# Optimization experiments

Measured on AMD Instinct MI355X. Metric: run time of the kernel, lower is better.

## Reference

```python
import jax, jax.numpy as jnp
import numpy as np
import math

DIM_Q = 512; DIM_K = 512; DIM_V = 512; H = 8; EPS = 1e-5

def _layernorm(x, g, b):
    mu = jnp.mean(x, axis=-1, keepdims=True)
    var = jnp.mean((x - mu) ** 2, axis=-1, keepdims=True)
    return (x - mu) * jax.lax.rsqrt(var + EPS) * g + b

def setup_inputs() -> dict:
    key = jax.random.key(0)
    ks = jax.random.split(key, 12)
    B, NQ, NK = 8, 1024, 1024
    s = 0.02
    return {
        "Q": jax.random.normal(ks[0], (B, NQ, DIM_Q), jnp.float32),
        "K": jax.random.normal(ks[1], (B, NK, DIM_K), jnp.float32),
        "attention_mask": jax.random.randint(ks[2], (B, NK), 0, 2, jnp.int32),
        "Wq": jax.random.normal(ks[3], (DIM_Q, DIM_V), jnp.float32) * s,
        "bq": jnp.zeros((DIM_V,), jnp.float32),
        "Wk": jax.random.normal(ks[4], (DIM_K, DIM_V), jnp.float32) * s,
        "bk": jnp.zeros((DIM_V,), jnp.float32),
        "Wv": jax.random.normal(ks[5], (DIM_K, DIM_V), jnp.float32) * s,
        "bv": jnp.zeros((DIM_V,), jnp.float32),
        "Wo": jax.random.normal(ks[6], (DIM_V, DIM_V), jnp.float32) * s,
        "bo": jnp.zeros((DIM_V,), jnp.float32),
        "g0": jnp.ones((DIM_V,), jnp.float32),
        "b0": jnp.zeros((DIM_V,), jnp.float32),
        "g1": jnp.ones((DIM_V,), jnp.float32),
        "b1": jnp.zeros((DIM_V,), jnp.float32),
    }

def reference(Q, K, attention_mask, Wq, bq, Wk, bk, Wv, bv, Wo, bo, g0, b0, g1, b1):
    B, NQ, _ = Q.shape
    NK = K.shape[1]
    dh = DIM_V // H
    q = (Q @ Wq + bq).reshape(B, NQ, H, dh).transpose(0, 2, 1, 3)  # (B,H,NQ,dh)
    k = (K @ Wk + bk).reshape(B, NK, H, dh).transpose(0, 2, 1, 3)
    v = (K @ Wv + bv).reshape(B, NK, H, dh).transpose(0, 2, 1, 3)
    # NOTE: original scales by sqrt(dim_V), not sqrt(head_dim)
    scores = jnp.einsum("bhqd,bhkd->bhqk", q, k) / math.sqrt(DIM_V)
    scores = jnp.where(attention_mask[:, None, None, :] == 0, -10000.0, scores)
    A = jax.nn.softmax(scores, axis=-1)
    o = q + jnp.einsum("bhqk,bhkd->bhqd", A, v)  # residual before output proj
    O = o.transpose(0, 2, 1, 3).reshape(B, NQ, DIM_V)
    O = _layernorm(O, g0, b0)
    O = O + jax.nn.relu(O @ Wo + bo)
    O = _layernorm(O, g1, b1)
    return O
```

## Files before the change

kernel.cpp:

```cpp
#include <hip/hip_runtime.h>
#include <hip/hip_bf16.h>

typedef __attribute__((ext_vector_type(8))) short short8;
typedef __attribute__((ext_vector_type(4))) short short4v;
typedef __attribute__((ext_vector_type(4))) float float4v;
typedef __attribute__((ext_vector_type(4))) unsigned uint4v;

#define LDT 72
#define SCALE 0.044194173824159216f

__device__ inline unsigned short f2b(float f) {
    return __builtin_bit_cast(unsigned short, __float2bfloat16(f));
}
__device__ inline float b2f(unsigned short s) {
    return __uint_as_float(((unsigned)s) << 16);
}
__device__ inline unsigned pk2(float lo, float hi) {
    return (unsigned)f2b(lo) | ((unsigned)f2b(hi) << 16);
}

__global__ void cast_bf16_kernel(const float* __restrict__ in,
                                 unsigned short* __restrict__ out, int n) {
    int i = (blockIdx.x * blockDim.x + threadIdx.x) * 8;
    if (i < n) {
        float4v a = *(const float4v*)(in + i);
        float4v b = *(const float4v*)(in + i + 4);
        uint4v o = {pk2(a[0], a[1]), pk2(a[2], a[3]), pk2(b[0], b[1]), pk2(b[2], b[3])};
        *(uint4v*)(out + i) = o;
    }
}

__global__ void transpose_w_kernel(const float* __restrict__ W0, const float* __restrict__ W1,
                                   const float* __restrict__ W2, const float* __restrict__ W3,
                                   unsigned short* __restrict__ out) {
    const float* W = (blockIdx.z == 0) ? W0 : (blockIdx.z == 1) ? W1
                   : (blockIdx.z == 2) ? W2 : W3;
    unsigned short* o = out + (size_t)blockIdx.z * 512 * 512;
    __shared__ float tile[32][33];
    int k0 = blockIdx.x * 32, n0 = blockIdx.y * 32;
    int tx = threadIdx.x & 31, ty = threadIdx.x >> 5;
    for (int r = ty; r < 32; r += 8) tile[r][tx] = W[(size_t)(k0 + r) * 512 + n0 + tx];
    __syncthreads();
    for (int r = ty; r < 32; r += 8) o[(size_t)(n0 + r) * 512 + k0 + tx] = f2b(tile[tx][r]);
}

__global__ __launch_bounds__(256) void gemm_kernel(
    const unsigned short* __restrict__ Qb, const unsigned short* __restrict__ Kb,
    const unsigned short* __restrict__ hb, const unsigned short* __restrict__ WT,
    const float* __restrict__ bq, const float* __restrict__ bk,
    const float* __restrict__ bv, const float* __restrict__ bo,
    unsigned short* __restrict__ qo, unsigned short* __restrict__ ko,
    unsigned short* __restrict__ vTo, unsigned short* __restrict__ to_,
    int zbase) {
    int z = zbase + blockIdx.z;
    const unsigned short* A = (z == 0) ? Qb : (z == 3) ? hb : Kb;
    const unsigned short* BT = WT + (size_t)z * 512 * 512;
    const float* bias = (z == 0) ? bq : (z == 1) ? bk : (z == 2) ? bv : bo;

    __shared__ unsigned short As[128 * LDT];
    __shared__ unsigned short Bs[128 * LDT];

    int tid = threadIdx.x;
    int lane = tid & 63, wave = tid >> 6;
    int wr = wave >> 1, wc = wave & 1;
    int l15 = lane & 15, lg = lane >> 4;
    int row0 = blockIdx.x * 128, col0 = blockIdx.y * 128;

    float4v acc[4][4];
#pragma unroll
    for (int m = 0; m < 4; m++)
#pragma unroll
        for (int n = 0; n < 4; n++) acc[m][n] = (float4v){0.f, 0.f, 0.f, 0.f};

    int sr = tid >> 3, sc = (tid & 7) * 8;

    for (int k0 = 0; k0 < 512; k0 += 64) {
        __syncthreads();
#pragma unroll
        for (int i = 0; i < 4; i++) {
            int r = sr + 32 * i;
            *(short8*)(As + r * LDT + sc) =
                *(const short8*)(A + (size_t)(row0 + r) * 512 + k0 + sc);
            *(short8*)(Bs + r * LDT + sc) =
                *(const short8*)(BT + (size_t)(col0 + r) * 512 + k0 + sc);
        }
        __syncthreads();
#pragma unroll
        for (int kk = 0; kk < 2; kk++) {
            short8 af[4], bf[4];
#pragma unroll
            for (int m = 0; m < 4; m++)
                af[m] = *(const short8*)(As + (wr * 64 + m * 16 + l15) * LDT + kk * 32 + lg * 8);
#pragma unroll
            for (int n = 0; n < 4; n++)
                bf[n] = *(const short8*)(Bs + (wc * 64 + n * 16 + l15) * LDT + kk * 32 + lg * 8);
#pragma unroll
            for (int m = 0; m < 4; m++)
#pragma unroll
                for (int n = 0; n < 4; n++)
                    acc[m][n] = __builtin_amdgcn_mfma_f32_16x16x32_bf16(af[m], bf[n], acc[m][n], 0, 0, 0);
        }
    }

#pragma unroll
    for (int n = 0; n < 4; n++) {
        int col = col0 + wc * 64 + n * 16 + l15;
        float bias_v = bias[col];
#pragma unroll
        for (int m = 0; m < 4; m++) {
            int rowb = row0 + wr * 64 + m * 16 + lg * 4;
            float4v v = acc[m][n];
            if (z == 2) {
                int b = rowb >> 10, tq = rowb & 1023;
                int h = col >> 6, d = col & 63;
                short4v st;
#pragma unroll
                for (int r = 0; r < 4; r++) st[r] = (short)f2b(v[r] + bias_v);
                *(short4v*)(vTo + ((((size_t)b * 8 + h) * 64 + d) << 10) + tq) = st;
            } else if (z == 3) {
#pragma unroll
                for (int r = 0; r < 4; r++) {
                    size_t idx = (size_t)(rowb + r) * 512 + col;
                    float x = v[r] + bias_v;
                    x = x > 0.f ? x : 0.f;
                    to_[idx] = f2b(x + b2f(hb[idx]));
                }
            } else {
                unsigned short* o = (z == 0) ? qo : ko;
#pragma unroll
                for (int r = 0; r < 4; r++)
                    o[(size_t)(rowb + r) * 512 + col] = f2b(v[r] + bias_v);
            }
        }
    }
}

__global__ __launch_bounds__(256) void attn_kernel(
    const unsigned short* __restrict__ qb, const unsigned short* __restrict__ kb,
    const unsigned short* __restrict__ vT, const int* __restrict__ mask,
    unsigned short* __restrict__ ob) {
    __shared__ unsigned short Ks[64 * LDT];
    __shared__ unsigned short Vs[64 * LDT];
    __shared__ float mbias[64];

    int tid = threadIdx.x;
    int lane = tid & 63, wave = tid >> 6;
    int l15 = lane & 15, lg = lane >> 4;
    int bh = blockIdx.y;
    int b = bh >> 3, h = bh & 7;
    int qrow0 = b * 1024 + blockIdx.x * 64 + wave * 16;

    short8 qf[2];
#pragma unroll
    for (int kk = 0; kk < 2; kk++)
        qf[kk] = *(const short8*)(qb + (size_t)(qrow0 + l15) * 512 + h * 64 + kk * 32 + lg * 8);

    float m_run = -1e30f, l_run = 0.f;
    float4v oacc[4];
#pragma unroll
    for (int n = 0; n < 4; n++) oacc[n] = (float4v){0.f, 0.f, 0.f, 0.f};

    int stok = tid >> 2, scoff = (tid & 3) * 16;
    int prow = (stok & 0x23) | ((stok & 4) << 2) | ((stok & 0x18) >> 1);

    for (int jt = 0; jt < 16; jt++) {
        __syncthreads();
        {
            const unsigned short* kg =
                kb + (size_t)(b * 1024 + jt * 64 + stok) * 512 + h * 64 + scoff;
            *(short8*)(Ks + prow * LDT + scoff) = *(const short8*)kg;
            *(short8*)(Ks + prow * LDT + scoff + 8) = *(const short8*)(kg + 8);
            const unsigned short* vg =
                vT + (((size_t)bh * 64 + stok) << 10) + jt * 64 + scoff;
            *(short8*)(Vs + stok * LDT + scoff) = *(const short8*)vg;
            *(short8*)(Vs + stok * LDT + scoff + 8) = *(const short8*)(vg + 8);
            if (tid < 64) mbias[tid] = mask[b * 1024 + jt * 64 + tid] ? 0.f : -10000.f;
        }
        __syncthreads();

        float p[4][4];
#pragma unroll
        for (int jf = 0; jf < 4; jf++) {
            short8 kf0 = *(const short8*)(Ks + (jf * 16 + l15) * LDT + lg * 8);
            short8 kf1 = *(const short8*)(Ks + (jf * 16 + l15) * LDT + 32 + lg * 8);
            float4v t = (float4v){0.f, 0.f, 0.f, 0.f};
            t = __builtin_amdgcn_mfma_f32_16x16x32_bf16(kf0, qf[0], t, 0, 0, 0);
            t = __builtin_amdgcn_mfma_f32_16x16x32_bf16(kf1, qf[1], t, 0, 0, 0);
#pragma unroll
            for (int r = 0; r < 4; r++) p[jf][r] = t[r];
        }
        float mx = -1e30f;
#pragma unroll
        for (int jf = 0; jf < 4; jf++)
#pragma unroll
            for (int r = 0; r < 4; r++) {
                float val = fmaf(p[jf][r], SCALE,
                                 mbias[32 * (jf >> 1) + 8 * lg + 4 * (jf & 1) + r]);
                p[jf][r] = val;
                mx = fmaxf(mx, val);
            }
        mx = fmaxf(mx, __shfl_xor(mx, 16));
        mx = fmaxf(mx, __shfl_xor(mx, 32));
        float mnew = fmaxf(m_run, mx);
        float sf = __expf(m_run - mnew);
        m_run = mnew;
        float ps = 0.f;
#pragma unroll
        for (int jf = 0; jf < 4; jf++)
#pragma unroll
            for (int r = 0; r < 4; r++) {
                float e = __expf(p[jf][r] - mnew);
                p[jf][r] = e;
                ps += e;
            }
        ps += __shfl_xor(ps, 16);
        ps += __shfl_xor(ps, 32);
        l_run = l_run * sf + ps;
#pragma unroll
        for (int n = 0; n < 4; n++)
#pragma unroll
            for (int r = 0; r < 4; r++) oacc[n][r] *= sf;

        uint4v w0 = {pk2(p[0][0], p[0][1]), pk2(p[0][2], p[0][3]),
                     pk2(p[1][0], p[1][1]), pk2(p[1][2], p[1][3])};
        uint4v w1 = {pk2(p[2][0], p[2][1]), pk2(p[2][2], p[2][3]),
                     pk2(p[3][0], p[3][1]), pk2(p[3][2], p[3][3])};
        short8 pb0 = __builtin_bit_cast(short8, w0);
        short8 pb1 = __builtin_bit_cast(short8, w1);

#pragma unroll
        for (int n = 0; n < 4; n++) {
            short8 vf0 = *(const short8*)(Vs + (n * 16 + l15) * LDT + lg * 8);
            short8 vf1 = *(const short8*)(Vs + (n * 16 + l15) * LDT + 32 + lg * 8);
            oacc[n] = __builtin_amdgcn_mfma_f32_16x16x32_bf16(vf0, pb0, oacc[n], 0, 0, 0);
            oacc[n] = __builtin_amdgcn_mfma_f32_16x16x32_bf16(vf1, pb1, oacc[n], 0, 0, 0);
        }
    }

    float inv = 1.f / l_run;
#pragma unroll
    for (int n = 0; n < 4; n++) {
        size_t base = (size_t)(qrow0 + l15) * 512 + h * 64 + n * 16 + lg * 4;
        short4v qr = *(const short4v*)(qb + base);
        short4v st;
#pragma unroll
        for (int r = 0; r < 4; r++)
            st[r] = (short)f2b(b2f((unsigned short)qr[r]) + oacc[n][r] * inv);
        *(short4v*)(ob + base) = st;
    }
}

__global__ void ln_kernel_bf16(const unsigned short* __restrict__ in,
                               const float* __restrict__ g, const float* __restrict__ bb,
                               unsigned short* __restrict__ out) {
    int row = blockIdx.x, lane = threadIdx.x;
    short8 v = *(const short8*)(in + (size_t)row * 512 + lane * 8);
    float x[8], s = 0.f, s2 = 0.f;
#pragma unroll
    for (int j = 0; j < 8; j++) {
        x[j] = b2f((unsigned short)v[j]);
        s += x[j];
        s2 += x[j] * x[j];
    }
#pragma unroll
    for (int off = 1; off < 64; off <<= 1) {
        s += __shfl_xor(s, off);
        s2 += __shfl_xor(s2, off);
    }
    float mu = s * (1.f / 512.f);
    float var = s2 * (1.f / 512.f) - mu * mu;
    float rs = rsqrtf(var + 1e-5f);
#pragma unroll
    for (int j = 0; j < 8; j++) {
        int c = lane * 8 + j;
        out[(size_t)row * 512 + c] = f2b((x[j] - mu) * rs * g[c] + bb[c]);
    }
}

__global__ void ln_kernel_f32(const unsigned short* __restrict__ in,
                              const float* __restrict__ g, const float* __restrict__ bb,
                              float* __restrict__ out) {
    int row = blockIdx.x, lane = threadIdx.x;
    short8 v = *(const short8*)(in + (size_t)row * 512 + lane * 8);
    float x[8], s = 0.f, s2 = 0.f;
#pragma unroll
    for (int j = 0; j < 8; j++) {
        x[j] = b2f((unsigned short)v[j]);
        s += x[j];
        s2 += x[j] * x[j];
    }
#pragma unroll
    for (int off = 1; off < 64; off <<= 1) {
        s += __shfl_xor(s, off);
        s2 += __shfl_xor(s2, off);
    }
    float mu = s * (1.f / 512.f);
    float var = s2 * (1.f / 512.f) - mu * mu;
    float rs = rsqrtf(var + 1e-5f);
#pragma unroll
    for (int j = 0; j < 8; j++) {
        int c = lane * 8 + j;
        out[(size_t)row * 512 + c] = (x[j] - mu) * rs * g[c] + bb[c];
    }
}

extern "C" void kernel_launch(void* const* d_in, const int* in_sizes, int n_in,
                              void* d_out, int out_size, void* d_ws, size_t ws_size,
                              hipStream_t stream) {
    const float* Q = (const float*)d_in[0];
    const float* K = (const float*)d_in[1];
    const int* mask = (const int*)d_in[2];
    const float* Wq = (const float*)d_in[3];
    const float* bq = (const float*)d_in[4];
    const float* Wk = (const float*)d_in[5];
    const float* bk = (const float*)d_in[6];
    const float* Wv = (const float*)d_in[7];
    const float* bv = (const float*)d_in[8];
    const float* Wo = (const float*)d_in[9];
    const float* bo = (const float*)d_in[10];
    const float* g0 = (const float*)d_in[11];
    const float* b0 = (const float*)d_in[12];
    const float* g1 = (const float*)d_in[13];
    const float* b1 = (const float*)d_in[14];
    float* out = (float*)d_out;

    const size_t N = 8192ull * 512;
    unsigned short* w16 = (unsigned short*)d_ws;
    unsigned short* Qb = w16;
    unsigned short* Kb = Qb + N;
    unsigned short* WT = Kb + N;
    unsigned short* qb = WT + 4ull * 512 * 512;
    unsigned short* kb = qb + N;
    unsigned short* vTb = kb + N;
    unsigned short* obuf = vTb + N;
    unsigned short* hbuf = obuf + N;
    unsigned short* tbuf = hbuf + N;

    cast_bf16_kernel<<<2048, 256, 0, stream>>>(Q, Qb, (int)N);
    cast_bf16_kernel<<<2048, 256, 0, stream>>>(K, Kb, (int)N);
    transpose_w_kernel<<<dim3(16, 16, 4), 256, 0, stream>>>(Wq, Wk, Wv, Wo, WT);
    gemm_kernel<<<dim3(64, 4, 3), 256, 0, stream>>>(Qb, Kb, hbuf, WT, bq, bk, bv, bo,
                                                    qb, kb, vTb, tbuf, 0);
    attn_kernel<<<dim3(16, 64), 256, 0, stream>>>(qb, kb, vTb, mask, obuf);
    ln_kernel_bf16<<<8192, 64, 0, stream>>>(obuf, g0, b0, hbuf);
    gemm_kernel<<<dim3(64, 4, 1), 256, 0, stream>>>(Qb, Kb, hbuf, WT, bq, bk, bv, bo,
                                                    qb, kb, vTb, tbuf, 3);
    ln_kernel_f32<<<8192, 64, 0, stream>>>(tbuf, g1, b1, out);
}
```

Measured before the change: 211.1 us.

## Widen attention key tile to 128, use exp2 softmax with lazy rescaling

Each attention iteration now processes 128 keys instead of 64, halving the number of loop iterations and barriers and enlarging the K/V shared-memory tiles. The score scale and mask bias are premultiplied by log2(e) so the softmax can use exp2f. The running-max update and accumulator rescale are skipped unless some lane's new max exceeds the old one by more than 8 in log2 units. This trades more shared memory and registers per block, which may lower occupancy, for fewer syncs and less rescaling work. Skipping the rescale also lets unnormalized exponentials grow by up to 2^8, which adds some precision risk.

```diff
diff --git a/kernel.cpp b/kernel.cpp
--- a/kernel.cpp
+++ b/kernel.cpp
@@ -7,7 +7,11 @@
 typedef __attribute__((ext_vector_type(4))) unsigned uint4v;
 
 #define LDT 72
+#define LDK 72
+#define LDV 136
 #define SCALE 0.044194173824159216f
+#define SCALE2 0.06376540791556074f
+#define MBIAS2 -14426.950408889634f
 
 __device__ inline unsigned short f2b(float f) {
     return __builtin_bit_cast(unsigned short, __float2bfloat16(f));
@@ -139,9 +143,9 @@
     const unsigned short* __restrict__ qb, const unsigned short* __restrict__ kb,
     const unsigned short* __restrict__ vT, const int* __restrict__ mask,
     unsigned short* __restrict__ ob) {
-    __shared__ unsigned short Ks[64 * LDT];
-    __shared__ unsigned short Vs[64 * LDT];
-    __shared__ float mbias[64];
+    __shared__ unsigned short Ks[128 * LDK];
+    __shared__ unsigned short Vs[64 * LDV];
+    __shared__ float mbias[128];
 
     int tid = threadIdx.x;
     int lane = tid & 63, wave = tid >> 6;
@@ -160,29 +164,34 @@
 #pragma unroll
     for (int n = 0; n < 4; n++) oacc[n] = (float4v){0.f, 0.f, 0.f, 0.f};
 
-    int stok = tid >> 2, scoff = (tid & 3) * 16;
-    int prow = (stok & 0x23) | ((stok & 4) << 2) | ((stok & 0x18) >> 1);
-
-    for (int jt = 0; jt < 16; jt++) {
+    int stok = tid >> 1, skoff = (tid & 1) * 32;
+    int prow = (stok & 0x63) | ((stok & 4) << 2) | ((stok & 0x18) >> 1);
+    int svd = tid >> 2, svoff = (tid & 3) * 32;
+
+    for (int jt = 0; jt < 8; jt++) {
         __syncthreads();
         {
             const unsigned short* kg =
-                kb + (size_t)(b * 1024 + jt * 64 + stok) * 512 + h * 64 + scoff;
-            *(short8*)(Ks + prow * LDT + scoff) = *(const short8*)kg;
-            *(short8*)(Ks + prow * LDT + scoff + 8) = *(const short8*)(kg + 8);
+                kb + (size_t)(b * 1024 + jt * 128 + stok) * 512 + h * 64 + skoff;
+            *(short8*)(Ks + prow * LDK + skoff)      = *(const short8*)kg;
+            *(short8*)(Ks + prow * LDK + skoff + 8)  = *(const short8*)(kg + 8);
+            *(short8*)(Ks + prow * LDK + skoff + 16) = *(const short8*)(kg + 16);
+            *(short8*)(Ks + prow * LDK + skoff + 24) = *(const short8*)(kg + 24);
             const unsigned short* vg =
-                vT + (((size_t)bh * 64 + stok) << 10) + jt * 64 + scoff;
-            *(short8*)(Vs + stok * LDT + scoff) = *(const short8*)vg;
-            *(short8*)(Vs + stok * LDT + scoff + 8) = *(const short8*)(vg + 8);
-            if (tid < 64) mbias[tid] = mask[b * 1024 + jt * 64 + tid] ? 0.f : -10000.f;
+                vT + (((size_t)bh * 64 + svd) << 10) + jt * 128 + svoff;
+            *(short8*)(Vs + svd * LDV + svoff)      = *(const short8*)vg;
+            *(short8*)(Vs + svd * LDV + svoff + 8)  = *(const short8*)(vg + 8);
+            *(short8*)(Vs + svd * LDV + svoff + 16) = *(const short8*)(vg + 16);
+            *(short8*)(Vs + svd * LDV + svoff + 24) = *(const short8*)(vg + 24);
+            if (tid < 128) mbias[tid] = mask[b * 1024 + jt * 128 + tid] ? 0.f : MBIAS2;
         }
         __syncthreads();
 
-        float p[4][4];
-#pragma unroll
-        for (int jf = 0; jf < 4; jf++) {
-            short8 kf0 = *(const short8*)(Ks + (jf * 16 + l15) * LDT + lg * 8);
-            short8 kf1 = *(const short8*)(Ks + (jf * 16 + l15) * LDT + 32 + lg * 8);
+        float p[8][4];
+#pragma unroll
+        for (int jf = 0; jf < 8; jf++) {
+            short8 kf0 = *(const short8*)(Ks + (jf * 16 + l15) * LDK + lg * 8);
+            short8 kf1 = *(const short8*)(Ks + (jf * 16 + l15) * LDK + 32 + lg * 8);
             float4v t = (float4v){0.f, 0.f, 0.f, 0.f};
             t = __builtin_amdgcn_mfma_f32_16x16x32_bf16(kf0, qf[0], t, 0, 0, 0);
             t = __builtin_amdgcn_mfma_f32_16x16x32_bf16(kf1, qf[1], t, 0, 0, 0);
@@ -191,50 +200,55 @@
         }
         float mx = -1e30f;
 #pragma unroll
-        for (int jf = 0; jf < 4; jf++)
+        for (int jf = 0; jf < 8; jf++)
 #pragma unroll
             for (int r = 0; r < 4; r++) {
-                float val = fmaf(p[jf][r], SCALE,
+                float val = fmaf(p[jf][r], SCALE2,
                                  mbias[32 * (jf >> 1) + 8 * lg + 4 * (jf & 1) + r]);
                 p[jf][r] = val;
                 mx = fmaxf(mx, val);
             }
         mx = fmaxf(mx, __shfl_xor(mx, 16));
         mx = fmaxf(mx, __shfl_xor(mx, 32));
-        float mnew = fmaxf(m_run, mx);
-        float sf = __expf(m_run - mnew);
-        m_run = mnew;
+        if (!__all(mx <= m_run + 8.f)) {
+            float mnew = fmaxf(m_run, mx);
+            float sf = exp2f(m_run - mnew);
+            m_run = mnew;
+            l_run *= sf;
+#pragma unroll
+            for (int n = 0; n < 4; n++)
+#pragma unroll
+                for (int r = 0; r < 4; r++) oacc[n][r] *= sf;
+        }
         float ps = 0.f;
 #pragma unroll
-        for (int jf = 0; jf < 4; jf++)
+        for (int jf = 0; jf < 8; jf++)
 #pragma unroll
             for (int r = 0; r < 4; r++) {
-                float e = __expf(p[jf][r] - mnew);
+                float e = exp2f(p[jf][r] - m_run);
                 p[jf][r] = e;
                 ps += e;
             }
         ps += __shfl_xor(ps, 16);
         ps += __shfl_xor(ps, 32);
-        l_run = l_run * sf + ps;
+        l_run += ps;
+
+        short8 pb[4];
+#pragma unroll
+        for (int ks = 0; ks < 4; ks++) {
+            uint4v w = {pk2(p[2 * ks][0], p[2 * ks][1]), pk2(p[2 * ks][2], p[2 * ks][3]),
+                        pk2(p[2 * ks + 1][0], p[2 * ks + 1][1]),
+                        pk2(p[2 * ks + 1][2], p[2 * ks + 1][3])};
+            pb[ks] = __builtin_bit_cast(short8, w);
+        }
+
 #pragma unroll
         for (int n = 0; n < 4; n++)
 #pragma unroll
-            for (int r = 0; r < 4; r++) oacc[n][r] *= sf;
-
-        uint4v w0 = {pk2(p[0][0], p[0][1]), pk2(p[0][2], p[0][3]),
-                     pk2(p[1][0], p[1][1]), pk2(p[1][2], p[1][3])};
-        uint4v w1 = {pk2(p[2][0], p[2][1]), pk2(p[2][2], p[2][3]),
-                     pk2(p[3][0], p[3][1]), pk2(p[3][2], p[3][3])};
-        short8 pb0 = __builtin_bit_cast(short8, w0);
-        short8 pb1 = __builtin_bit_cast(short8, w1);
-
-#pragma unroll
-        for (int n = 0; n < 4; n++) {
-            short8 vf0 = *(const short8*)(Vs + (n * 16 + l15) * LDT + lg * 8);
-            short8 vf1 = *(const short8*)(Vs + (n * 16 + l15) * LDT + 32 + lg * 8);
-            oacc[n] = __builtin_amdgcn_mfma_f32_16x16x32_bf16(vf0, pb0, oacc[n], 0, 0, 0);
-            oacc[n] = __builtin_amdgcn_mfma_f32_16x16x32_bf16(vf1, pb1, oacc[n], 0, 0, 0);
-        }
+            for (int ks = 0; ks < 4; ks++) {
+                short8 vf = *(const short8*)(Vs + (n * 16 + l15) * LDV + ks * 32 + lg * 8);
+                oacc[n] = __builtin_amdgcn_mfma_f32_16x16x32_bf16(vf, pb[ks], oacc[n], 0, 0, 0);
+            }
     }
 
     float inv = 1.f / l_run;
```

New measurement: 207.4 us. About the same (-1.8%).
